# Kernel tuning notes

Measured on AMD Instinct MI355X. Metric: run time of the kernel, lower is better.

Reference implementation:

```python
import jax, jax.numpy as jnp
import numpy as np

M, IN, OUT = 8192, 4096, 4096
BLOCK_N, BLOCK_K = 128, 128
NB = IN // BLOCK_K  # 32 in-blocks
INT8_MAX = 127.0
EPS = 1e-6


def setup_inputs() -> dict:
    key = jax.random.key(0)
    k1, k2, k3, k4 = jax.random.split(key, 4)
    x = jax.random.normal(k1, (M, IN), dtype=jnp.float32)
    # pre-quantized int8 weights, layout [output_size, input_size]
    weight_q = jax.random.randint(k2, (OUT, IN), -128, 128, dtype=jnp.int8)
    # block-wise scales, kernel-ready layout [in_blocks, 1, output_size]
    weight_scale = (jax.random.uniform(k3, (NB, 1, OUT), dtype=jnp.float32) + 0.5) * 0.01
    bias = jax.random.normal(k4, (OUT,), dtype=jnp.float32)
    return {"x": x, "weight_q": weight_q, "weight_scale": weight_scale, "bias": bias}


def _quantize_activation(x):
    # dynamic per-token symmetric int8 quantization
    amax = jnp.max(jnp.abs(x), axis=-1, keepdims=True)          # [M, 1]
    x_scale = jnp.maximum(amax, EPS) / INT8_MAX                  # [M, 1]
    x_q = jnp.clip(jnp.round(x / x_scale), -128.0, 127.0)        # [M, IN]
    return x_q, x_scale


def reference(x, weight_q, weight_scale, bias):
    # x: [M, IN]; weight_q: [OUT, IN] int8; weight_scale: [NB, 1, OUT]; bias: [OUT]
    x_q, x_scale = _quantize_activation(x)
    # Dequantize weights block-wise along K: scale for column k, row n is
    # weight_scale[k // BLOCK_K, 0, n].
    ws = weight_scale[:, 0, :].T                                 # [OUT, NB]
    w_deq = (weight_q.astype(jnp.float32).reshape(OUT, NB, BLOCK_K)
             * ws[:, :, None]).reshape(OUT, IN)                  # [OUT, IN] fp32
    # quantized matmul + dequant by activation scale
    out = jnp.einsum('mk,nk->mn', x_q, w_deq) * x_scale          # [M, OUT]
    out = out + bias
    return out
```

## Files before the change

kernel.cpp:

```cpp
#include <hip/hip_runtime.h>
#include <cstdint>

#define M_DIM 8192
#define K_DIM 4096
#define N_DIM 4096
#define NBLK 32
#define BLK  128

typedef int   v4i __attribute__((ext_vector_type(4)));
typedef float v4f __attribute__((ext_vector_type(4)));

__device__ __forceinline__ void gload_lds16(const void* g, void* l) {
  __builtin_amdgcn_global_load_lds(
      (const __attribute__((address_space(1))) void*)g,
      (__attribute__((address_space(3))) void*)l, 16, 0, 0);
}

__global__ __launch_bounds__(256) void pack_w(
    const int* __restrict__ w32, int* __restrict__ w8) {
  const size_t i = (size_t)blockIdx.x * 256 + threadIdx.x;
  const int4 v = ((const int4*)w32)[i];
  w8[i] = (v.x & 255) | ((v.y & 255) << 8) | ((v.z & 255) << 16) | ((v.w & 255) << 24);
}

__global__ __launch_bounds__(256) void quant_rows(
    const float* __restrict__ x, int8_t* __restrict__ xq, float* __restrict__ xs) {
  const int row = blockIdx.x;
  const int tid = threadIdx.x;
  const float4* xr = (const float4*)(x + (size_t)row * K_DIM);

  float4 v[4];
  float amax = 0.f;
#pragma unroll
  for (int i = 0; i < 4; ++i) {
    v[i] = xr[i * 256 + tid];
    amax = fmaxf(amax, fmaxf(fmaxf(fabsf(v[i].x), fabsf(v[i].y)),
                             fmaxf(fabsf(v[i].z), fabsf(v[i].w))));
  }
#pragma unroll
  for (int off = 32; off > 0; off >>= 1)
    amax = fmaxf(amax, __shfl_xor(amax, off, 64));

  __shared__ float red[4];
  if ((tid & 63) == 0) red[tid >> 6] = amax;
  __syncthreads();
  amax = fmaxf(fmaxf(red[0], red[1]), fmaxf(red[2], red[3]));
  amax = fmaxf(amax, 1e-6f);
  const float s   = amax / 127.0f;
  const float inv = 127.0f / amax;
  if (tid == 0) xs[row] = s;

  int* xqo = (int*)(xq + (size_t)row * K_DIM);
#pragma unroll
  for (int i = 0; i < 4; ++i) {
    int q0 = (int)fminf(fmaxf(rintf(v[i].x * inv), -128.f), 127.f);
    int q1 = (int)fminf(fmaxf(rintf(v[i].y * inv), -128.f), 127.f);
    int q2 = (int)fminf(fmaxf(rintf(v[i].z * inv), -128.f), 127.f);
    int q3 = (int)fminf(fmaxf(rintf(v[i].w * inv), -128.f), 127.f);
    xqo[i * 256 + tid] =
        (q0 & 255) | ((q1 & 255) << 8) | ((q2 & 255) << 16) | ((q3 & 255) << 24);
  }
}

__global__ __launch_bounds__(256) void gemm_q8(
    const int8_t* __restrict__ xq, const int8_t* __restrict__ wq,
    const float* __restrict__ wscale, const float* __restrict__ xs,
    const float* __restrict__ bias, float* __restrict__ out) {
  __shared__ int8_t lA[128 * 128];
  __shared__ int8_t lB[128 * 128];

  const int tid = threadIdx.x;
  const int m0 = blockIdx.x * 128;
  const int n0 = blockIdx.y * 128;

  const int srow   = tid >> 3;
  const int schunk = (tid & 7) ^ (srow & 7);
  const int8_t* ga = xq + (size_t)(m0 + srow) * K_DIM + schunk * 16;
  const int8_t* gb = wq + (size_t)(n0 + srow) * K_DIM + schunk * 16;
  int8_t* la_dst = lA + tid * 16;
  int8_t* lb_dst = lB + tid * 16;

  const int lane = tid & 63;
  const int wv = tid >> 6;
  const int wm = (wv & 1) << 6;
  const int wn = (wv >> 1) << 6;
  const int lr = lane & 15;
  const int lq = lane >> 4;

  int a_off[4][2], b_off[4][2];
#pragma unroll
  for (int h = 0; h < 2; ++h) {
    const int ch = (h << 2) | lq;
#pragma unroll
    for (int i = 0; i < 4; ++i) {
      const int rowA = wm + i * 16 + lr;
      a_off[i][h] = rowA * 128 + ((ch ^ (rowA & 7)) << 4);
    }
#pragma unroll
    for (int j = 0; j < 4; ++j) {
      const int rowB = wn + j * 16 + lr;
      b_off[j][h] = rowB * 128 + ((ch ^ (rowB & 7)) << 4);
    }
  }

  v4f facc[4][4];
#pragma unroll
  for (int i = 0; i < 4; ++i)
#pragma unroll
    for (int j = 0; j < 4; ++j) facc[i][j] = {0.f, 0.f, 0.f, 0.f};

  const float* wsp = wscale + n0 + wn + lr;

  for (int kb = 0; kb < NBLK; ++kb) {
    float wsv[4];
#pragma unroll
    for (int j = 0; j < 4; ++j) wsv[j] = wsp[(size_t)kb * N_DIM + j * 16];

    __syncthreads();
#pragma unroll
    for (int p = 0; p < 4; ++p) {
      gload_lds16(ga + (size_t)p * 32 * K_DIM, la_dst + p * 4096);
      gload_lds16(gb + (size_t)p * 32 * K_DIM, lb_dst + p * 4096);
    }
    ga += BLK;
    gb += BLK;
    __syncthreads();

    v4i af[4][2];
#pragma unroll
    for (int i = 0; i < 4; ++i)
#pragma unroll
      for (int h = 0; h < 2; ++h) af[i][h] = *(const v4i*)(lA + a_off[i][h]);

#pragma unroll
    for (int j = 0; j < 4; ++j) {
      const v4i b0 = *(const v4i*)(lB + b_off[j][0]);
      const v4i b1 = *(const v4i*)(lB + b_off[j][1]);
      v4i ic[4];
#pragma unroll
      for (int i = 0; i < 4; ++i) {
        ic[i] = {0, 0, 0, 0};
        ic[i] = __builtin_amdgcn_mfma_i32_16x16x64_i8(af[i][0], b0, ic[i], 0, 0, 0);
        ic[i] = __builtin_amdgcn_mfma_i32_16x16x64_i8(af[i][1], b1, ic[i], 0, 0, 0);
      }
#pragma unroll
      for (int i = 0; i < 4; ++i)
#pragma unroll
        for (int r = 0; r < 4; ++r)
          facc[i][j][r] += wsv[j] * (float)ic[i][r];
    }
  }

  float bv[4];
#pragma unroll
  for (int j = 0; j < 4; ++j) bv[j] = bias[n0 + wn + j * 16 + lr];
#pragma unroll
  for (int i = 0; i < 4; ++i) {
    const int mb = m0 + wm + i * 16 + (lq << 2);
#pragma unroll
    for (int r = 0; r < 4; ++r) {
      const float sc = xs[mb + r];
      float* op = out + (size_t)(mb + r) * N_DIM + n0 + wn + lr;
#pragma unroll
      for (int j = 0; j < 4; ++j) op[j * 16] = facc[i][j][r] * sc + bv[j];
    }
  }
}

extern "C" void kernel_launch(void* const* d_in, const int* in_sizes, int n_in,
                              void* d_out, int out_size, void* d_ws, size_t ws_size,
                              hipStream_t stream) {
  const float* x      = (const float*)d_in[0];
  const int*   w32    = (const int*)d_in[1];
  const float* wscale = (const float*)d_in[2];
  const float* bias   = (const float*)d_in[3];
  float* out = (float*)d_out;

  int8_t* xq  = (int8_t*)d_ws;
  int8_t* wq8 = (int8_t*)d_ws + (size_t)M_DIM * K_DIM;
  float*  xs  = (float*)((char*)d_ws + (size_t)M_DIM * K_DIM + (size_t)N_DIM * K_DIM);

  pack_w<<<(N_DIM * (size_t)K_DIM / 4 + 255) / 256, 256, 0, stream>>>(w32, (int*)wq8);
  quant_rows<<<M_DIM, 256, 0, stream>>>(x, xq, xs);
  dim3 grid(M_DIM / 128, N_DIM / 128);
  gemm_q8<<<grid, 256, 0, stream>>>(xq, wq8, wscale, xs, bias, out);
}
```

Measured before the change: 460.8 us.

## Enlarge GEMM tile to 256x256 with double-buffered LDS prefetch pipeline

Raises the int8 GEMM block tile from 128x128 to 256x256 with 512 threads, so each wave computes a 128x64 sub-tile. LDS is double-buffered and the next K-tile is fetched straight into LDS while the current tile runs through MFMA, with sched barriers and setprio used to interleave loads and math. This targets the exposed global-load latency and the two full syncs per K step, and raises operand reuse per byte loaded. In exchange it uses 128KB of LDS per block (one block per CU) and more accumulator registers, which cuts occupancy, and the grid shrinks to 512 blocks.

After: 465.6 us. No clear change (+1.0%).

```diff
diff --git a/kernel.cpp b/kernel.cpp
--- a/kernel.cpp
+++ b/kernel.cpp
@@ -4,8 +4,7 @@
 #define M_DIM 8192
 #define K_DIM 4096
 #define N_DIM 4096
-#define NBLK 32
-#define BLK  128
+#define NKT   32
 
 typedef int   v4i __attribute__((ext_vector_type(4)));
 typedef float v4f __attribute__((ext_vector_type(4)));
@@ -62,100 +61,131 @@
   }
 }
 
-__global__ __launch_bounds__(256) void gemm_q8(
+__global__ __launch_bounds__(512, 2) void gemm_q8(
     const int8_t* __restrict__ xq, const int8_t* __restrict__ wq,
     const float* __restrict__ wscale, const float* __restrict__ xs,
     const float* __restrict__ bias, float* __restrict__ out) {
-  __shared__ int8_t lA[128 * 128];
-  __shared__ int8_t lB[128 * 128];
+  __shared__ int8_t lA[2][32768];
+  __shared__ int8_t lB[2][32768];
 
   const int tid = threadIdx.x;
-  const int m0 = blockIdx.x * 128;
-  const int n0 = blockIdx.y * 128;
+  const int m0 = blockIdx.x * 256;
+  const int n0 = blockIdx.y * 256;
 
   const int srow   = tid >> 3;
   const int schunk = (tid & 7) ^ (srow & 7);
   const int8_t* ga = xq + (size_t)(m0 + srow) * K_DIM + schunk * 16;
   const int8_t* gb = wq + (size_t)(n0 + srow) * K_DIM + schunk * 16;
-  int8_t* la_dst = lA + tid * 16;
-  int8_t* lb_dst = lB + tid * 16;
 
   const int lane = tid & 63;
   const int wv = tid >> 6;
-  const int wm = (wv & 1) << 6;
-  const int wn = (wv >> 1) << 6;
+  const int wm = (wv >> 2) << 7;
+  const int wn = (wv & 3) << 6;
   const int lr = lane & 15;
   const int lq = lane >> 4;
 
-  int a_off[4][2], b_off[4][2];
-#pragma unroll
-  for (int h = 0; h < 2; ++h) {
-    const int ch = (h << 2) | lq;
-#pragma unroll
-    for (int i = 0; i < 4; ++i) {
-      const int rowA = wm + i * 16 + lr;
-      a_off[i][h] = rowA * 128 + ((ch ^ (rowA & 7)) << 4);
+  const int swz0 = ((lq ^ (lr & 7)) << 4);
+  const int swz1 = (((4 | lq) ^ (lr & 7)) << 4);
+  const int arow = (wm + lr) << 7;
+  const int brow = (wn + lr) << 7;
+
+  v4f facc[8][4];
+#pragma unroll
+  for (int i = 0; i < 8; ++i)
+#pragma unroll
+    for (int j = 0; j < 4; ++j) facc[i][j] = {0.f, 0.f, 0.f, 0.f};
+
+  const float* wsp = wscale + n0 + wn + lr;
+
+#pragma unroll
+  for (int h = 0; h < 2; ++h)
+#pragma unroll
+    for (int p = 0; p < 2; ++p) {
+      const size_t go = (size_t)(h * 128 + p * 64) * K_DIM;
+      const int lo = h * 16384 + p * 8192 + tid * 16;
+      gload_lds16(ga + go, &lA[0][lo]);
+      gload_lds16(gb + go, &lB[0][lo]);
     }
-#pragma unroll
-    for (int j = 0; j < 4; ++j) {
-      const int rowB = wn + j * 16 + lr;
-      b_off[j][h] = rowB * 128 + ((ch ^ (rowB & 7)) << 4);
+  asm volatile("s_waitcnt vmcnt(0)" ::: "memory");
+  __builtin_amdgcn_s_barrier();
+
+  for (int kt = 0; kt < NKT; ++kt) {
+    const int d = kt & 1;
+    const int kn = (kt + 1) & (NKT - 1);
+    const int8_t* gan = ga + (size_t)kn * 128;
+    const int8_t* gbn = gb + (size_t)kn * 128;
+    int8_t* lan = &lA[d ^ 1][0];
+    int8_t* lbn = &lB[d ^ 1][0];
+    const int8_t* pa0 = &lA[d][arow + swz0];
+    const int8_t* pa1 = &lA[d][arow + swz1];
+    const int8_t* pb0 = &lB[d][brow + swz0];
+    const int8_t* pb1 = &lB[d][brow + swz1];
+
+    float wsv[4];
+#pragma unroll
+    for (int j = 0; j < 4; ++j) wsv[j] = wsp[(size_t)kt * N_DIM + j * 16];
+
+#pragma unroll
+    for (int q = 0; q < 4; ++q) {
+      v4i af[2][2], bf[4][2];
+#pragma unroll
+      for (int ii = 0; ii < 2; ++ii) {
+        af[ii][0] = *(const v4i*)(pa0 + (q * 2 + ii) * 2048);
+        af[ii][1] = *(const v4i*)(pa1 + (q * 2 + ii) * 2048);
+      }
+#pragma unroll
+      for (int j = 0; j < 4; ++j) {
+        bf[j][0] = *(const v4i*)(pb0 + j * 2048);
+        bf[j][1] = *(const v4i*)(pb1 + j * 2048);
+      }
+
+      if (q < 2) {
+#pragma unroll
+        for (int p = 0; p < 2; ++p) {
+          const size_t go = (size_t)(q * 128 + p * 64) * K_DIM;
+          const int lo = q * 16384 + p * 8192 + tid * 16;
+          gload_lds16(gan + go, lan + lo);
+          gload_lds16(gbn + go, lbn + lo);
+        }
+      }
+
+      __builtin_amdgcn_s_barrier();
+      asm volatile("s_waitcnt lgkmcnt(0)" ::: "memory");
+      __builtin_amdgcn_sched_barrier(0);
+
+      __builtin_amdgcn_s_setprio(1);
+      v4i ic[2][4];
+#pragma unroll
+      for (int ii = 0; ii < 2; ++ii)
+#pragma unroll
+        for (int j = 0; j < 4; ++j) {
+          ic[ii][j] = {0, 0, 0, 0};
+          ic[ii][j] = __builtin_amdgcn_mfma_i32_16x16x64_i8(af[ii][0], bf[j][0], ic[ii][j], 0, 0, 0);
+          ic[ii][j] = __builtin_amdgcn_mfma_i32_16x16x64_i8(af[ii][1], bf[j][1], ic[ii][j], 0, 0, 0);
+        }
+      __builtin_amdgcn_s_setprio(0);
+
+#pragma unroll
+      for (int ii = 0; ii < 2; ++ii)
+#pragma unroll
+        for (int j = 0; j < 4; ++j)
+#pragma unroll
+          for (int r = 0; r < 4; ++r)
+            facc[q * 2 + ii][j][r] += wsv[j] * (float)ic[ii][j][r];
+
+      if (q == 3) {
+        asm volatile("s_waitcnt vmcnt(0)" ::: "memory");
+        __builtin_amdgcn_sched_barrier(0);
+      }
+      __builtin_amdgcn_s_barrier();
     }
   }
 
-  v4f facc[4][4];
-#pragma unroll
-  for (int i = 0; i < 4; ++i)
-#pragma unroll
-    for (int j = 0; j < 4; ++j) facc[i][j] = {0.f, 0.f, 0.f, 0.f};
-
-  const float* wsp = wscale + n0 + wn + lr;
-
-  for (int kb = 0; kb < NBLK; ++kb) {
-    float wsv[4];
-#pragma unroll
-    for (int j = 0; j < 4; ++j) wsv[j] = wsp[(size_t)kb * N_DIM + j * 16];
-
-    __syncthreads();
-#pragma unroll
-    for (int p = 0; p < 4; ++p) {
-      gload_lds16(ga + (size_t)p * 32 * K_DIM, la_dst + p * 4096);
-      gload_lds16(gb + (size_t)p * 32 * K_DIM, lb_dst + p * 4096);
-    }
-    ga += BLK;
-    gb += BLK;
-    __syncthreads();
-
-    v4i af[4][2];
-#pragma unroll
-    for (int i = 0; i < 4; ++i)
-#pragma unroll
-      for (int h = 0; h < 2; ++h) af[i][h] = *(const v4i*)(lA + a_off[i][h]);
-
-#pragma unroll
-    for (int j = 0; j < 4; ++j) {
-      const v4i b0 = *(const v4i*)(lB + b_off[j][0]);
-      const v4i b1 = *(const v4i*)(lB + b_off[j][1]);
-      v4i ic[4];
-#pragma unroll
-      for (int i = 0; i < 4; ++i) {
-        ic[i] = {0, 0, 0, 0};
-        ic[i] = __builtin_amdgcn_mfma_i32_16x16x64_i8(af[i][0], b0, ic[i], 0, 0, 0);
-        ic[i] = __builtin_amdgcn_mfma_i32_16x16x64_i8(af[i][1], b1, ic[i], 0, 0, 0);
-      }
-#pragma unroll
-      for (int i = 0; i < 4; ++i)
-#pragma unroll
-        for (int r = 0; r < 4; ++r)
-          facc[i][j][r] += wsv[j] * (float)ic[i][r];
-    }
-  }
-
   float bv[4];
 #pragma unroll
   for (int j = 0; j < 4; ++j) bv[j] = bias[n0 + wn + j * 16 + lr];
 #pragma unroll
-  for (int i = 0; i < 4; ++i) {
+  for (int i = 0; i < 8; ++i) {
     const int mb = m0 + wm + i * 16 + (lq << 2);
 #pragma unroll
     for (int r = 0; r < 4; ++r) {
@@ -182,6 +212,6 @@
 
   pack_w<<<(N_DIM * (size_t)K_DIM / 4 + 255) / 256, 256, 0, stream>>>(w32, (int*)wq8);
   quant_rows<<<M_DIM, 256, 0, stream>>>(x, xq, xs);
-  dim3 grid(M_DIM / 128, N_DIM / 128);
-  gemm_q8<<<grid, 256, 0, stream>>>(xq, wq8, wscale, xs, bias, out);
-}
+  dim3 grid(M_DIM / 256, N_DIM / 256);
+  gemm_q8<<<grid, 512, 0, stream>>>(xq, wq8, wscale, xs, bias, out);
+}
```
